# Kernel tuning notes

Measured on AMD Instinct MI355X. Metric: run time of the kernel, lower is better.

The kernel has to match this reference:

```python
import jax, jax.numpy as jnp
import numpy as np

C = 256; CM = 8; MAXI = 100; NCLS = 80
KP = (CM + 2) * CM + CM + CM * CM + CM + CM + 1  # 169 dynamic-kernel params

def _ln(x, g, b, eps=1e-5):
    m = x.mean(-1, keepdims=True)
    v = ((x - m) ** 2).mean(-1, keepdims=True)
    return g * (x - m) * jax.lax.rsqrt(v + eps) + b

def _mlp(x, hw, hb, lng, lnb, fw, fb):
    # torchvision MLP: [Linear -> LayerNorm -> SiLU] * n_hidden -> Linear
    for i in range(hw.shape[0]):
        x = jax.nn.silu(_ln(x @ hw[i] + hb[i], lng[i], lnb[i]))
    return x @ fw + fb

def _conv1x1_bn(x, w, s, b):
    # 1x1 conv (no bias) + inference-mode BatchNorm folded into per-channel affine
    y = jnp.einsum('bchw,oc->bohw', x, w)
    return y * s[None, :, None, None] + b[None, :, None, None]

def _grid(h, w):
    # normalized cell-center coordinates, (x, y) order, shape [h, w, 2]
    ys = (jnp.arange(h, dtype=jnp.float32) + 0.5) / h
    xs = (jnp.arange(w, dtype=jnp.float32) + 0.5) / w
    return jnp.stack([jnp.broadcast_to(xs[None, :], (h, w)),
                      jnp.broadcast_to(ys[:, None], (h, w))], axis=-1)

def setup_inputs() -> dict:
    key = jax.random.key(0)
    ks = iter(jax.random.split(key, 40))
    nrm = lambda shape, s=0.02: s * jax.random.normal(next(ks), shape, jnp.float32)
    B = 4
    inp = {
        'x0': jax.random.normal(next(ks), (B, 3, 512, 512), jnp.float32),
        'x1': jax.random.normal(next(ks), (B, 64, 256, 256), jnp.float32),
        'x2': jax.random.normal(next(ks), (B, 128, 128, 128), jnp.float32),
        'x3': jax.random.normal(next(ks), (B, 256, 64, 64), jnp.float32),
        'x4': jax.random.normal(next(ks), (B, 512, 32, 32), jnp.float32),
        'x5': jax.random.normal(next(ks), (B, 1024, 16, 16), jnp.float32),
        'lat3_w': nrm((C, 256)), 'lat3_s': jnp.ones((C,)), 'lat3_b': jnp.zeros((C,)),
        'lat4_w': nrm((C, 512)), 'lat4_s': jnp.ones((C,)), 'lat4_b': jnp.zeros((C,)),
        'lat5_w': nrm((C, 1024)), 'lat5_s': jnp.ones((C,)), 'lat5_b': jnp.zeros((C,)),
        'mlat_w': nrm((C, 256)), 'mlat_s': jnp.ones((C,)), 'mlat_b': jnp.zeros((C,)),
        'mhead_w': nrm((CM, C, 3, 3)), 'mhead_s': jnp.ones((CM,)), 'mhead_b': jnp.zeros((CM,)),
        'loc_hw': nrm((4, C, C)), 'loc_hb': jnp.zeros((4, C)), 'loc_lng': jnp.ones((4, C)), 'loc_lnb': jnp.zeros((4, C)),
        'loc_fw': nrm((C, 1)), 'loc_fb': -5.0 * jnp.ones((1,)),
        'cls_hw': nrm((4, C, C)), 'cls_hb': jnp.zeros((4, C)), 'cls_lng': jnp.ones((4, C)), 'cls_lnb': jnp.zeros((4, C)),
        'cls_fw': nrm((C, NCLS)), 'cls_fb': jnp.zeros((NCLS,)),
        'ker_hw': nrm((4, C, C)), 'ker_hb': jnp.zeros((4, C)), 'ker_lng': jnp.ones((4, C)), 'ker_lnb': jnp.zeros((4, C)),
        'ker_fw': nrm((C, KP)), 'ker_fb': jnp.zeros((KP,)),
    }
    return inp

def reference(x0, x1, x2, x3, x4, x5,
              lat3_w, lat3_s, lat3_b, lat4_w, lat4_s, lat4_b, lat5_w, lat5_s, lat5_b,
              mlat_w, mlat_s, mlat_b, mhead_w, mhead_s, mhead_b,
              loc_hw, loc_hb, loc_lng, loc_lnb, loc_fw, loc_fb,
              cls_hw, cls_hb, cls_lng, cls_lnb, cls_fw, cls_fb,
              ker_hw, ker_hb, ker_lng, ker_lnb, ker_fw, ker_fb):
    B, _, H, W = x0.shape
    lvls = [(x3, lat3_w, lat3_s, lat3_b), (x4, lat4_w, lat4_s, lat4_b), (x5, lat5_w, lat5_s, lat5_b)]
    feats = [_conv1x1_bn(x, w, s, b) for (x, w, s, b) in lvls]
    flat = jnp.concatenate([f.reshape(B, C, -1).transpose(0, 2, 1) for f in feats], axis=1)  # [B, L, C]
    loc_logits = _mlp(flat, loc_hw, loc_hb, loc_lng, loc_lnb, loc_fw, loc_fb)[..., 0]       # [B, L]
    top_vals, top_idx = jax.lax.top_k(loc_logits, MAXI)
    scores = jax.nn.sigmoid(top_vals)
    num_instances = (scores > 0.5).sum(axis=1)
    gfeat = jnp.take_along_axis(flat, top_idx[:, :, None], axis=1)  # [B, I, C]
    # mask branch
    mf = _conv1x1_bn(x3, mlat_w, mlat_s, mlat_b)
    mf = jax.lax.conv_general_dilated(mf, mhead_w, (1, 1), 'SAME', dimension_numbers=('NCHW', 'OIHW', 'NCHW'))
    mf = jax.nn.silu(mf * mhead_s[None, :, None, None] + mhead_b[None, :, None, None])  # [B, CM, h3, w3]
    h3, w3 = x3.shape[2], x3.shape[3]
    offs_flat = jnp.concatenate([_grid(x.shape[2], x.shape[3]).reshape(-1, 2) for x in (x3, x4, x5)], axis=0)
    offs = offs_flat[top_idx]                                # [B, I, 2]
    grid = _grid(h3, w3).transpose(2, 0, 1)                  # [2, h3, w3]
    grid = grid[None, None] - offs[:, :, :, None, None]      # [B, I, 2, h, w]
    mfi = jnp.broadcast_to(mf[:, None], (B, MAXI, CM, h3, w3))
    feats_i = jnp.concatenate([mfi, grid], axis=2)           # [B, I, CM+2, h, w]
    dyn = _mlp(gfeat, ker_hw, ker_hb, ker_lng, ker_lnb, ker_fw, ker_fb)  # [B, I, KP]
    c = CM
    o = (c + 2) * c
    w1 = dyn[..., :o].reshape(B, MAXI, c + 2, c)
    b1 = dyn[..., o:o + c].reshape(B, MAXI, c, 1, 1); o += c
    w2 = dyn[..., o:o + c * c].reshape(B, MAXI, c, c); o += c * c
    b2 = dyn[..., o:o + c].reshape(B, MAXI, c, 1, 1); o += c
    w3 = dyn[..., o:o + c].reshape(B, MAXI, c, 1); o += c
    b3 = dyn[..., o:].reshape(B, MAXI, 1, 1, 1)
    m = jax.nn.silu(jnp.einsum('bichw,bicd->bidhw', feats_i, w1) + b1)
    m = jax.nn.silu(jnp.einsum('bichw,bicd->bidhw', m, w2) + b2)
    m = jnp.einsum('bichw,bicd->bidhw', m, w3) + b3
    masks = jax.nn.sigmoid(m[:, :, 0])                       # [B, I, h3, w3]
    classes = jnp.argmax(_mlp(gfeat, cls_hw, cls_hb, cls_lng, cls_lnb, cls_fw, cls_fb), axis=-1)
    masks = jax.image.resize(masks, (B, MAXI, H, W), method='bilinear', antialias=False)
    return (num_instances, scores, classes, masks)
```

## Files before the change

kernel.cpp:

```cpp
#include <hip/hip_runtime.h>
#include <hip/hip_bf16.h>
#include <math.h>

#define DEVI __device__ __forceinline__

constexpr int LTOT  = 5376;
constexpr int NINST = 100;
constexpr int NCLS  = 80;
constexpr int KPAR  = 169;

DEVI float waveAllSum(float v) {
#pragma unroll
  for (int s = 32; s > 0; s >>= 1) v += __shfl_xor(v, s, 64);
  return v;
}
DEVI float siluf(float x) { return x / (1.0f + expf(-x)); }
DEVI float sigmf(float x) { return 1.0f / (1.0f + expf(-x)); }

__global__ __launch_bounds__(256) void wtrans(
    const float* __restrict__ w3, const float* __restrict__ w4,
    const float* __restrict__ w5, const float* __restrict__ wm,
    float* __restrict__ wt3, float* __restrict__ wt4,
    float* __restrict__ wt5, float* __restrict__ wtm)
{
  __shared__ float t[64][65];
  const int bid = blockIdx.x;
  const float* src; float* dst; int K, rel;
  if (bid < 16)       { src = w3; dst = wt3; K = 256;  rel = bid; }
  else if (bid < 48)  { src = w4; dst = wt4; K = 512;  rel = bid - 16; }
  else if (bid < 112) { src = w5; dst = wt5; K = 1024; rel = bid - 48; }
  else                { src = wm; dst = wtm; K = 256;  rel = bid - 112; }
  const int ctiles = K >> 6;
  const int ot = rel / ctiles, ct = rel % ctiles;
  const int o0 = ot * 64, c0 = ct * 64;
  const int tid = threadIdx.x;
#pragma unroll
  for (int s = 0; s < 16; ++s) {
    const int e = tid + 256*s;
    const int r = e >> 6, c = e & 63;
    t[r][c] = src[(long)(o0 + r)*K + c0 + c];
  }
  __syncthreads();
#pragma unroll
  for (int s = 0; s < 16; ++s) {
    const int e = tid + 256*s;
    const int q = e >> 6, p = e & 63;
    dst[(long)(c0 + q)*256 + o0 + p] = t[p][q];
  }
}

__global__ __launch_bounds__(256) void lateral_main(
    const float* __restrict__ x3, const float* __restrict__ x4, const float* __restrict__ x5,
    const float* __restrict__ wt3, const float* __restrict__ s3, const float* __restrict__ b3,
    const float* __restrict__ wt4, const float* __restrict__ s4, const float* __restrict__ b4,
    const float* __restrict__ wt5, const float* __restrict__ s5, const float* __restrict__ b5,
    const float* __restrict__ wtm, const float* __restrict__ sm, const float* __restrict__ bm,
    float* __restrict__ flat, float* __restrict__ mlatb)
{
  __shared__ float xs[32][36];
  __shared__ float ws[32][256];
  const int tid = threadIdx.x;
  const int rg = tid >> 6, cg = tid & 63;
  const int bid = blockIdx.x;
  const float *x, *wt, *sc, *bi;
  int K, P, b, p0, baseL = 0; bool tomlat = false;
  if (bid < 512)       { x=x3; wt=wt3; sc=s3; bi=b3; K=256;  P=4096; b=bid>>7;  p0=(bid&127)*32; }
  else if (bid < 1024) { const int rel=bid-512;  x=x3; wt=wtm; sc=sm; bi=bm; K=256;  P=4096; b=rel>>7; p0=(rel&127)*32; tomlat=true; }
  else if (bid < 1152) { const int rel=bid-1024; x=x4; wt=wt4; sc=s4; bi=b4; K=512;  P=1024; b=rel>>5; p0=(rel&31)*32; baseL=4096; }
  else                 { const int rel=bid-1152; x=x5; wt=wt5; sc=s5; bi=b5; K=1024; P=256;  b=rel>>3; p0=(rel&7)*32;  baseL=5120; }
  const float* xb = x + (long)b * K * P;
  float acc[8][4] = {};
  const int nkb = K >> 5;
  for (int kb = 0; kb < nkb; ++kb) {
    __syncthreads();
#pragma unroll
    for (int s = 0; s < 4; ++s) {
      const int e = tid + 256*s;
      const int kk = e >> 5, px = e & 31;
      xs[kk][px] = xb[(long)(kb*32 + kk)*P + p0 + px];
    }
    {
      const float4* w4p = reinterpret_cast<const float4*>(wt + (kb << 13));
#pragma unroll
      for (int q = 0; q < 8; ++q) {
        const int c = tid + (q << 8);
        *reinterpret_cast<float4*>(&ws[c >> 6][4*(c & 63)]) = w4p[c];
      }
    }
    __syncthreads();
#pragma unroll
    for (int kk = 0; kk < 32; ++kk) {
      const float4 a0 = *reinterpret_cast<const float4*>(&xs[kk][8*rg]);
      const float4 a1 = *reinterpret_cast<const float4*>(&xs[kk][8*rg+4]);
      const float ar[8] = {a0.x,a0.y,a0.z,a0.w,a1.x,a1.y,a1.z,a1.w};
      const float4 wv = *reinterpret_cast<const float4*>(&ws[kk][4*cg]);
#pragma unroll
      for (int i = 0; i < 8; ++i) {
        acc[i][0] += ar[i]*wv.x; acc[i][1] += ar[i]*wv.y;
        acc[i][2] += ar[i]*wv.z; acc[i][3] += ar[i]*wv.w;
      }
    }
  }
  const float4 sA = *reinterpret_cast<const float4*>(&sc[4*cg]);
  const float4 bA = *reinterpret_cast<const float4*>(&bi[4*cg]);
  if (!tomlat) {
#pragma unroll
    for (int i = 0; i < 8; ++i) {
      const float4 ov = { acc[i][0]*sA.x+bA.x, acc[i][1]*sA.y+bA.y,
                          acc[i][2]*sA.z+bA.z, acc[i][3]*sA.w+bA.w };
      *reinterpret_cast<float4*>(&flat[((long)b*LTOT + baseL + p0 + 8*rg + i)*256 + 4*cg]) = ov;
    }
  } else {
#pragma unroll
    for (int j = 0; j < 4; ++j) {
      const float sj = (&sA.x)[j], bj = (&bA.x)[j];
      const float4 o0 = { acc[0][j]*sj+bj, acc[1][j]*sj+bj, acc[2][j]*sj+bj, acc[3][j]*sj+bj };
      const float4 o1 = { acc[4][j]*sj+bj, acc[5][j]*sj+bj, acc[6][j]*sj+bj, acc[7][j]*sj+bj };
      float* mb = &mlatb[((long)b*256 + 4*cg + j)*4096 + p0 + 8*rg];
      *reinterpret_cast<float4*>(mb) = o0;
      *reinterpret_cast<float4*>(mb + 4) = o1;
    }
  }
}

__global__ __attribute__((amdgpu_waves_per_eu(3, 3))) __launch_bounds__(256)
void loc4(
    const float* __restrict__ in, const float* __restrict__ hw,
    const float* __restrict__ hb, const float* __restrict__ lng, const float* __restrict__ lnb,
    const float* __restrict__ fw, const float* __restrict__ fb, float* __restrict__ logits)
{
  __shared__ float xls[4][7][256];
  const int tid = threadIdx.x;
  const int rg = tid >> 6, cg = tid & 63;
  const int r0 = blockIdx.x * 28 + rg * 7;
  float* xw = &xls[rg][0][0];
#pragma unroll
  for (int i = 0; i < 7; ++i) {
    const float4 v = *reinterpret_cast<const float4*>(&in[(long)(r0 + i)*256 + 4*cg]);
    *reinterpret_cast<float4*>(&xw[i*256 + 4*cg]) = v;
  }
  const float4 fw4 = *reinterpret_cast<const float4*>(&fw[4*cg]);
  const float fbv = fb[0];

#define LOADG(W, A, g)                                                      \
  {                                                                         \
    const int kk4 = (g) << 2;                                               \
    W[0] = *reinterpret_cast<const float4*>(&w[(kk4 + 0) << 8]);            \
    W[1] = *reinterpret_cast<const float4*>(&w[(kk4 + 1) << 8]);            \
    W[2] = *reinterpret_cast<const float4*>(&w[(kk4 + 2) << 8]);            \
    W[3] = *reinterpret_cast<const float4*>(&w[(kk4 + 3) << 8]);            \
    _Pragma("unroll")                                                       \
    for (int r = 0; r < 7; ++r)                                             \
      A[r] = *reinterpret_cast<const float4*>(&xw[r*256 + kk4]);            \
  }
#define FMAG(W, A)                                                          \
  _Pragma("unroll")                                                         \
  for (int u = 0; u < 4; ++u) {                                             \
    _Pragma("unroll")                                                       \
    for (int r = 0; r < 7; ++r) {                                           \
      const float a = (&A[r].x)[u];                                         \
      acc[r][0] += a*W[u].x; acc[r][1] += a*W[u].y;                         \
      acc[r][2] += a*W[u].z; acc[r][3] += a*W[u].w;                         \
    }                                                                       \
  }

  for (int L = 0; L < 4; ++L) {
    const float* w = hw + L*65536 + 4*cg;
    float acc[7][4] = {};
    float4 wvA[4], wvB[4], avA[7], avB[7];
    LOADG(wvA, avA, 0)
    for (int g = 0; g < 64; g += 2) {
      LOADG(wvB, avB, g + 1)
      FMAG(wvA, avA)
      if (g + 2 < 64) LOADG(wvA, avA, g + 2)
      FMAG(wvB, avB)
    }
    const float4 hb4 = *reinterpret_cast<const float4*>(&hb[L*256 + 4*cg]);
    const float4 g4  = *reinterpret_cast<const float4*>(&lng[L*256 + 4*cg]);
    const float4 lb4 = *reinterpret_cast<const float4*>(&lnb[L*256 + 4*cg]);
#pragma unroll
    for (int r = 0; r < 7; ++r) {
      const float y0 = acc[r][0]+hb4.x, y1 = acc[r][1]+hb4.y;
      const float y2 = acc[r][2]+hb4.z, y3 = acc[r][3]+hb4.w;
      const float m = waveAllSum(y0+y1+y2+y3) * (1.0f/256.0f);
      const float d0=y0-m, d1=y1-m, d2=y2-m, d3=y3-m;
      const float var = waveAllSum(d0*d0+d1*d1+d2*d2+d3*d3) * (1.0f/256.0f);
      const float rs = rsqrtf(var + 1e-5f);
      const float o0 = siluf(g4.x*d0*rs + lb4.x);
      const float o1 = siluf(g4.y*d1*rs + lb4.y);
      const float o2 = siluf(g4.z*d2*rs + lb4.z);
      const float o3 = siluf(g4.w*d3*rs + lb4.w);
      if (L < 3) {
        const float4 ov = {o0, o1, o2, o3};
        *reinterpret_cast<float4*>(&xw[r*256 + 4*cg]) = ov;
      } else {
        float d = o0*fw4.x + o1*fw4.y + o2*fw4.z + o3*fw4.w;
        d = waveAllSum(d);
        if (cg == 0) logits[r0 + r] = d + fbv;
      }
    }
  }
#undef LOADG
#undef FMAG
}

__global__ __launch_bounds__(256) void topk_gather(
    const float* __restrict__ logits, const float* __restrict__ flat,
    int* __restrict__ topi, float* __restrict__ gfeat,
    float* __restrict__ dout)
{
  __shared__ float sv[LTOT];
  __shared__ float rv[4];
  __shared__ int   ri[4];
  __shared__ int   sidx[NINST];
  __shared__ int   winsh;
  const int b = blockIdx.x, tid = threadIdx.x;
  for (int l = tid; l < LTOT; l += 256) sv[l] = logits[b*LTOT + l];
  __syncthreads();
  float bvt = -INFINITY; int bit = 0x7fffffff;
  for (int l = tid; l < LTOT; l += 256) {
    const float v = sv[l];
    if (v > bvt) { bvt = v; bit = l; }
  }
  int cnt = 0;
  for (int t = 0; t < NINST; ++t) {
    float bv = bvt; int bidx = bit;
#pragma unroll
    for (int s = 32; s > 0; s >>= 1) {
      const float v2 = __shfl_xor(bv, s, 64);
      const int   i2 = __shfl_xor(bidx, s, 64);
      if (v2 > bv || (v2 == bv && i2 < bidx)) { bv = v2; bidx = i2; }
    }
    if ((tid & 63) == 0) { rv[tid >> 6] = bv; ri[tid >> 6] = bidx; }
    __syncthreads();
    if (tid == 0) {
      bv = rv[0]; bidx = ri[0];
#pragma unroll
      for (int q = 1; q < 4; ++q)
        if (rv[q] > bv || (rv[q] == bv && ri[q] < bidx)) { bv = rv[q]; bidx = ri[q]; }
      sidx[t] = bidx; topi[b*NINST + t] = bidx;
      dout[4 + b*NINST + t] = sigmf(bv);
      if (bv > 0.0f) ++cnt;
      winsh = bidx;
    }
    __syncthreads();
    const int wi = winsh;
    if (bit == wi) {
      sv[wi] = -INFINITY;
      bvt = -INFINITY; bit = 0x7fffffff;
      for (int l = tid; l < LTOT; l += 256) {
        const float v = sv[l];
        if (v > bvt) { bvt = v; bit = l; }
      }
    }
  }
  if (tid == 0) dout[b] = (float)cnt;
  __syncthreads();
  for (int t = 0; t < NINST; ++t) {
    const int ix = sidx[t];
    gfeat[((long)b*NINST + t)*256 + tid] = flat[((long)b*LTOT + ix)*256 + tid];
  }
}

__global__ __launch_bounds__(256) void clsker4(
    const float* __restrict__ gfeat, float* __restrict__ h2,
    const float* __restrict__ chw, const float* __restrict__ chb,
    const float* __restrict__ cg_, const float* __restrict__ cb_,
    const float* __restrict__ khw, const float* __restrict__ khb,
    const float* __restrict__ kg_, const float* __restrict__ kb_)
{
  __shared__ float xls[4][2][256];
  const int tid = threadIdx.x;
  const int rg = tid >> 6, cg = tid & 63;
  const bool ker = blockIdx.x >= 50;
  const int rb = (ker ? (blockIdx.x - 50) : blockIdx.x) * 8;
  const int r0 = rb + 2*rg;
  const int ob = r0 + (ker ? 400 : 0);
  const float* hw = ker ? khw : chw;
  const float* hb = ker ? khb : chb;
  const float* g_ = ker ? kg_ : cg_;
  const float* lb = ker ? kb_ : cb_;
  float* xw = &xls[rg][0][0];
#pragma unroll
  for (int i = 0; i < 2; ++i) {
    const float4 v = *reinterpret_cast<const float4*>(&gfeat[(long)(r0 + i)*256 + 4*cg]);
    *reinterpret_cast<float4*>(&xw[i*256 + 4*cg]) = v;
  }

#define LOADG2(W, A, g)                                                     \
  {                                                                         \
    const int kk4 = (g) << 2;                                               \
    W[0] = *reinterpret_cast<const float4*>(&w[(kk4 + 0) << 8]);            \
    W[1] = *reinterpret_cast<const float4*>(&w[(kk4 + 1) << 8]);            \
    W[2] = *reinterpret_cast<const float4*>(&w[(kk4 + 2) << 8]);            \
    W[3] = *reinterpret_cast<const float4*>(&w[(kk4 + 3) << 8]);            \
    A[0] = *reinterpret_cast<const float4*>(&xw[kk4]);                      \
    A[1] = *reinterpret_cast<const float4*>(&xw[256 + kk4]);                \
  }
#define FMAG2(W, A)                                                         \
  _Pragma("unroll")                                                         \
  for (int u = 0; u < 4; ++u) {                                             \
    _Pragma("unroll")                                                       \
    for (int r = 0; r < 2; ++r) {                                           \
      const float a = (&A[r].x)[u];                                         \
      acc[r][0] += a*W[u].x; acc[r][1] += a*W[u].y;                         \
      acc[r][2] += a*W[u].z; acc[r][3] += a*W[u].w;                         \
    }                                                                       \
  }

  for (int L = 0; L < 4; ++L) {
    const float* w = hw + L*65536 + 4*cg;
    float acc[2][4] = {};
    float4 wvA[4], wvB[4], avA[2], avB[2];
    LOADG2(wvA, avA, 0)
    for (int g = 0; g < 64; g += 2) {
      LOADG2(wvB, avB, g + 1)
      FMAG2(wvA, avA)
      if (g + 2 < 64) LOADG2(wvA, avA, g + 2)
      FMAG2(wvB, avB)
    }
    const float4 hb4 = *reinterpret_cast<const float4*>(&hb[L*256 + 4*cg]);
    const float4 g4  = *reinterpret_cast<const float4*>(&g_[L*256 + 4*cg]);
    const float4 lb4 = *reinterpret_cast<const float4*>(&lb[L*256 + 4*cg]);
#pragma unroll
    for (int i = 0; i < 2; ++i) {
      const float y0 = acc[i][0]+hb4.x, y1 = acc[i][1]+hb4.y;
      const float y2 = acc[i][2]+hb4.z, y3 = acc[i][3]+hb4.w;
      const float m = waveAllSum(y0+y1+y2+y3) * (1.0f/256.0f);
      const float d0=y0-m, d1=y1-m, d2=y2-m, d3=y3-m;
      const float var = waveAllSum(d0*d0+d1*d1+d2*d2+d3*d3) * (1.0f/256.0f);
      const float rs = rsqrtf(var + 1e-5f);
      const float4 ov = { siluf(g4.x*d0*rs + lb4.x), siluf(g4.y*d1*rs + lb4.y),
                          siluf(g4.z*d2*rs + lb4.z), siluf(g4.w*d3*rs + lb4.w) };
      if (L < 3) *reinterpret_cast<float4*>(&xw[i*256 + 4*cg]) = ov;
      else       *reinterpret_cast<float4*>(&h2[(long)(ob + i)*256 + 4*cg]) = ov;
    }
  }
#undef LOADG2
#undef FMAG2
}

__global__ __launch_bounds__(256) void heads(
    const float* __restrict__ h2, const float* __restrict__ cfw, const float* __restrict__ cfb,
    const float* __restrict__ kfw, const float* __restrict__ kfb,
    float* __restrict__ dout, float* __restrict__ dyn)
{
  __shared__ float xr[256];
  __shared__ float lv[NCLS];
  const int bid = blockIdx.x, tid = threadIdx.x;
  xr[tid] = h2[(long)bid*256 + tid];
  __syncthreads();
  if (bid < 400) {
    if (tid < NCLS) {
      float a0=0.f, a1=0.f, a2=0.f, a3=0.f;
      for (int k = 0; k < 256; k += 4) {
        a0 += xr[k+0]*cfw[(k+0)*NCLS + tid];
        a1 += xr[k+1]*cfw[(k+1)*NCLS + tid];
        a2 += xr[k+2]*cfw[(k+2)*NCLS + tid];
        a3 += xr[k+3]*cfw[(k+3)*NCLS + tid];
      }
      lv[tid] = (a0+a1) + (a2+a3) + cfb[tid];
    }
    __syncthreads();
    if (tid == 0) {
      float bv = lv[0]; int bi2 = 0;
      for (int o = 1; o < NCLS; ++o) if (lv[o] > bv) { bv = lv[o]; bi2 = o; }
      dout[404 + bid] = (float)bi2;
    }
  } else {
    if (tid < KPAR) {
      float a0=0.f, a1=0.f, a2=0.f, a3=0.f;
      for (int k = 0; k < 256; k += 4) {
        a0 += xr[k+0]*kfw[(k+0)*KPAR + tid];
        a1 += xr[k+1]*kfw[(k+1)*KPAR + tid];
        a2 += xr[k+2]*kfw[(k+2)*KPAR + tid];
        a3 += xr[k+3]*kfw[(k+3)*KPAR + tid];
      }
      dyn[(long)(bid-400)*KPAR + tid] = (a0+a1) + (a2+a3) + kfb[tid];
    }
  }
}

__global__ __launch_bounds__(256) void conv3(
    const float* __restrict__ mlat, const float* __restrict__ mw,
    float* __restrict__ partial)
{
  const int bid = blockIdx.x;
  const int cc = bid & 7;
  const int tile = (bid >> 3) & 15;
  const int b = bid >> 7;
  const int y0 = (tile >> 2)*16, x0 = (tile & 3)*16;
  const int tid = threadIdx.x;
  const int ly = tid >> 4, lx = tid & 15;
  __shared__ float til[2][18][19];
  __shared__ float wch[8][32][12];
  for (int e = tid; e < 2304; e += 256) {
    const int o = e / 288, rem = e % 288;
    const int c = rem / 9, qq = rem - c*9;
    wch[o][c][qq] = mw[((o*256) + cc*32 + c)*9 + qq];
  }
  int lofs[3], gofs[3], chn[3]; bool vld[3], has[3];
  float* tf = &til[0][0][0];
#pragma unroll
  for (int s = 0; s < 3; ++s) {
    const int e = tid + 256*s;
    has[s] = (e < 648);
    lofs[s] = 0; gofs[s] = 0; chn[s] = 0; vld[s] = false;
    if (has[s]) {
      const int ch = (e >= 324) ? 1 : 0;
      const int pos = e - ch*324;
      const int iy = pos / 18, ix = pos - iy*18;
      const int gy = y0 - 1 + iy, gx = x0 - 1 + ix;
      vld[s] = (gy >= 0 && gy < 64 && gx >= 0 && gx < 64);
      lofs[s] = ch*342 + iy*19 + ix;
      gofs[s] = gy*64 + gx;
      chn[s] = ch;
    }
  }
  const float* xbase = mlat + ((long)b*256 + cc*32)*4096;
  float acc[8] = {};
  for (int r = 0; r < 16; ++r) {
    __syncthreads();
#pragma unroll
    for (int s = 0; s < 3; ++s)
      if (has[s]) tf[lofs[s]] = vld[s] ? xbase[(long)(2*r + chn[s])*4096 + gofs[s]] : 0.f;
    __syncthreads();
#pragma unroll
    for (int ch = 0; ch < 2; ++ch) {
      const int c = 2*r + ch;
      float t[9];
#pragma unroll
      for (int dy = 0; dy < 3; ++dy)
#pragma unroll
        for (int dx = 0; dx < 3; ++dx) t[dy*3+dx] = til[ch][ly+dy][lx+dx];
#pragma unroll
      for (int o = 0; o < 8; ++o) {
        const float4 wa = *reinterpret_cast<const float4*>(&wch[o][c][0]);
        const float4 wb = *reinterpret_cast<const float4*>(&wch[o][c][4]);
        const float w8 = wch[o][c][8];
        acc[o] += t[0]*wa.x + t[1]*wa.y + t[2]*wa.z + t[3]*wa.w
                + t[4]*wb.x + t[5]*wb.y + t[6]*wb.z + t[7]*wb.w + t[8]*w8;
      }
    }
  }
  const long pbase = (((long)b*8 + cc)*8)*4096 + (y0+ly)*64 + (x0+lx);
#pragma unroll
  for (int o = 0; o < 8; ++o) partial[pbase + (long)o*4096] = acc[o];
}

__global__ __launch_bounds__(256) void mhead_fin(
    const float* __restrict__ partial, const float* __restrict__ s,
    const float* __restrict__ bi, float* __restrict__ mhead)
{
  const int idx = blockIdx.x*256 + threadIdx.x;
  const int p = idx & 4095;
  const int o = (idx >> 12) & 7;
  const int b = idx >> 15;
  float v = 0.f;
#pragma unroll
  for (int cc = 0; cc < 8; ++cc) v += partial[(((long)b*8 + cc)*8 + o)*4096 + p];
  v = v*s[o] + bi[o];
  mhead[idx] = siluf(v);
}

__global__ __launch_bounds__(256) void mask_fused(
    const float* __restrict__ dyn, const int* __restrict__ topi,
    const float* __restrict__ mhead, float* __restrict__ dout)
{
  __shared__ float msrc[18][64];
  __shared__ float dd[KPAR];
  __shared__ float so[2];
  const int bid = blockIdx.x;
  const int inst = bid >> 2, q = bid & 3;
  const int tid = threadIdx.x;
  if (tid < KPAR) dd[tid] = dyn[(long)inst*KPAR + tid];
  if (tid == 0) {
    const int l = topi[inst];
    float ox, oy;
    if (l < 4096)      { ox = ((l & 63) + 0.5f)*(1.f/64.f); oy = ((l >> 6) + 0.5f)*(1.f/64.f); }
    else if (l < 5120) { const int t = l - 4096; ox = ((t & 31) + 0.5f)*(1.f/32.f); oy = ((t >> 5) + 0.5f)*(1.f/32.f); }
    else               { const int t = l - 5120; ox = ((t & 15) + 0.5f)*(1.f/16.f); oy = ((t >> 4) + 0.5f)*(1.f/16.f); }
    so[0] = ox; so[1] = oy;
  }
  __syncthreads();
  const float ox = so[0], oy = so[1];
  const int b = inst / NINST;
  const float* mh = mhead + (long)b*8*4096;
  const int r0s = 16*q - 1;
  for (int e = tid; e < 1152; e += 256) {
    const int r = e >> 6, x = e & 63;
    int sy = r0s + r; sy = sy < 0 ? 0 : (sy > 63 ? 63 : sy);
    const int p = sy*64 + x;
    float f[10];
#pragma unroll
    for (int c = 0; c < 8; ++c) f[c] = mh[c*4096 + p];
    f[8] = (x + 0.5f)*(1.f/64.f) - ox;
    f[9] = (sy + 0.5f)*(1.f/64.f) - oy;
    float m1[8];
#pragma unroll
    for (int d = 0; d < 8; ++d) {
      float t = dd[80 + d];
#pragma unroll
      for (int c = 0; c < 10; ++c) t += f[c]*dd[c*8 + d];
      m1[d] = siluf(t);
    }
    float m2[8];
#pragma unroll
    for (int d = 0; d < 8; ++d) {
      float t = dd[152 + d];
#pragma unroll
      for (int c = 0; c < 8; ++c) t += m1[c]*dd[88 + c*8 + d];
      m2[d] = siluf(t);
    }
    float o = dd[168];
#pragma unroll
    for (int c = 0; c < 8; ++c) o += m2[c]*dd[160 + c];
    msrc[r][x] = sigmf(o);
  }
  __syncthreads();
  const int j4 = tid & 127;
  const int half = tid >> 7;
  const int ix0 = (j4 & 1) ? (j4 >> 1) : (j4 >> 1) - 1;
  const int xlo = ix0 < 0 ? 0 : ix0;
  const int xhi = (ix0 + 1 > 63) ? 63 : ix0 + 1;
  float fx[4];
#pragma unroll
  for (int m = 0; m < 4; ++m) {
    const int x = 4*j4 + m;
    const float tx = (x + 0.5f)*0.125f - 0.5f;
    fx[m] = tx - (float)ix0;
  }
  float* dbase = dout + 804 + ((long)inst << 18);
  for (int it = 0; it < 64; ++it) {
    const int yy = 2*it + half;
    const int y = 128*q + yy;
    const float ty = (y + 0.5f)*0.125f - 0.5f;
    const float fyf = floorf(ty);
    const int iy0 = (int)fyf;
    const float fy = ty - fyf;
    const int r0 = iy0 - r0s;
    const float L0 = msrc[r0][xlo],   R0 = msrc[r0][xhi];
    const float L1 = msrc[r0+1][xlo], R1 = msrc[r0+1][xhi];
    const float L = L0 + (L1 - L0)*fy;
    const float R = R0 + (R1 - R0)*fy;
    const float4 ovv = { L + (R - L)*fx[0], L + (R - L)*fx[1],
                         L + (R - L)*fx[2], L + (R - L)*fx[3] };
    *reinterpret_cast<float4*>(&dbase[((long)y << 9) + (j4 << 2)]) = ovv;
  }
}

extern "C" void kernel_launch(void* const* d_in, const int* in_sizes, int n_in,
                              void* d_out, int out_size, void* d_ws, size_t ws_size,
                              hipStream_t stream)
{
  (void)in_sizes; (void)n_in; (void)out_size; (void)ws_size;
  const float* x3      = (const float*)d_in[3];
  const float* x4      = (const float*)d_in[4];
  const float* x5      = (const float*)d_in[5];
  const float* lat3_w  = (const float*)d_in[6];
  const float* lat3_s  = (const float*)d_in[7];
  const float* lat3_b  = (const float*)d_in[8];
  const float* lat4_w  = (const float*)d_in[9];
  const float* lat4_s  = (const float*)d_in[10];
  const float* lat4_b  = (const float*)d_in[11];
  const float* lat5_w  = (const float*)d_in[12];
  const float* lat5_s  = (const float*)d_in[13];
  const float* lat5_b  = (const float*)d_in[14];
  const float* mlat_w  = (const float*)d_in[15];
  const float* mlat_s  = (const float*)d_in[16];
  const float* mlat_b  = (const float*)d_in[17];
  const float* mhead_w = (const float*)d_in[18];
  const float* mhead_s = (const float*)d_in[19];
  const float* mhead_b = (const float*)d_in[20];
  const float* loc_hw  = (const float*)d_in[21];
  const float* loc_hb  = (const float*)d_in[22];
  const float* loc_lng = (const float*)d_in[23];
  const float* loc_lnb = (const float*)d_in[24];
  const float* loc_fw  = (const float*)d_in[25];
  const float* loc_fb  = (const float*)d_in[26];
  const float* cls_hw  = (const float*)d_in[27];
  const float* cls_hb  = (const float*)d_in[28];
  const float* cls_lng = (const float*)d_in[29];
  const float* cls_lnb = (const float*)d_in[30];
  const float* cls_fw  = (const float*)d_in[31];
  const float* cls_fb  = (const float*)d_in[32];
  const float* ker_hw  = (const float*)d_in[33];
  const float* ker_hb  = (const float*)d_in[34];
  const float* ker_lng = (const float*)d_in[35];
  const float* ker_lnb = (const float*)d_in[36];
  const float* ker_fw  = (const float*)d_in[37];
  const float* ker_fb  = (const float*)d_in[38];

  float* ws      = (float*)d_ws;
  float* flat    = ws;
  float* mlatb   = ws + 5505024;
  float* partial = ws + 9699328;
  float* mheadb  = ws + 10747904;
  float* h2      = ws + 10878976;
  float* logits  = ws + 11083776;
  int*   topi    = (int*)(ws + 11105280);
  float* gfeat   = ws + 11105680;
  float* dynb    = ws + 11208080;
  float* wt3     = ws + 11275680;
  float* wt4     = ws + 11341216;
  float* wt5     = ws + 11472288;
  float* wtm     = ws + 11734432;
  float* dout    = (float*)d_out;

  wtrans<<<128, 256, 0, stream>>>(lat3_w, lat4_w, lat5_w, mlat_w, wt3, wt4, wt5, wtm);
  lateral_main<<<1184, 256, 0, stream>>>(x3, x4, x5,
      wt3, lat3_s, lat3_b, wt4, lat4_s, lat4_b, wt5, lat5_s, lat5_b,
      wtm, mlat_s, mlat_b, flat, mlatb);
  conv3<<<512, 256, 0, stream>>>(mlatb, mhead_w, partial);
  mhead_fin<<<512, 256, 0, stream>>>(partial, mhead_s, mhead_b, mheadb);
  loc4<<<768, 256, 0, stream>>>(flat, loc_hw, loc_hb, loc_lng, loc_lnb,
                                loc_fw, loc_fb, logits);
  topk_gather<<<4, 256, 0, stream>>>(logits, flat, topi, gfeat, dout);
  clsker4<<<100, 256, 0, stream>>>(gfeat, h2,
      cls_hw, cls_hb, cls_lng, cls_lnb, ker_hw, ker_hb, ker_lng, ker_lnb);
  heads<<<800, 256, 0, stream>>>(h2, cls_fw, cls_fb, ker_fw, ker_fb, dout, dynb);
  mask_fused<<<1600, 256, 0, stream>>>(dynb, topi, mheadb, dout);
}
```

Before: 793.0 us.

## Fold mask lateral 1x1 conv+BN into 3x3 mask head weights

Precomputes combined weights by composing the mask lateral 1x1 conv and its BN affine into the 3x3 mask-head conv, so conv3 reads x3 directly. This removes the 512 lateral_main blocks that produced the mlat buffer, along with its write and read traffic. The folded BN bias is added in mhead_fin as a border-aware sum of per-tap biases, which keeps zero-padding semantics exact. It adds a small weight-prep step and a slight change in floating-point rounding order.

```diff
diff --git a/kernel.cpp b/kernel.cpp
--- a/kernel.cpp
+++ b/kernel.cpp
@@ -17,23 +17,37 @@
 DEVI float siluf(float x) { return x / (1.0f + expf(-x)); }
 DEVI float sigmf(float x) { return 1.0f / (1.0f + expf(-x)); }
 
-__global__ __launch_bounds__(256) void wtrans(
+__global__ __launch_bounds__(256) void wprep(
     const float* __restrict__ w3, const float* __restrict__ w4,
-    const float* __restrict__ w5, const float* __restrict__ wm,
-    float* __restrict__ wt3, float* __restrict__ wt4,
-    float* __restrict__ wt5, float* __restrict__ wtm)
+    const float* __restrict__ w5,
+    const float* __restrict__ mlat_w, const float* __restrict__ mlat_s,
+    const float* __restrict__ mlat_b, const float* __restrict__ mhead_w,
+    float* __restrict__ wt3, float* __restrict__ wt4, float* __restrict__ wt5,
+    float* __restrict__ wc, float* __restrict__ Bt)
 {
   __shared__ float t[64][65];
   const int bid = blockIdx.x;
+  const int tid = threadIdx.x;
+  if (bid >= 112) {
+    const int rel = bid - 112;
+    const int o = rel / 9, q = rel % 9;
+    float acc = 0.f, bacc = 0.f;
+    for (int c = 0; c < 256; ++c) {
+      const float mh = mhead_w[((o << 8) + c)*9 + q];
+      acc  += mh * mlat_s[c] * mlat_w[(c << 8) + tid];
+      bacc += mh * mlat_b[c];
+    }
+    wc[((o << 8) + tid)*9 + q] = acc;
+    if (tid == 0) Bt[rel] = bacc;
+    return;
+  }
   const float* src; float* dst; int K, rel;
   if (bid < 16)       { src = w3; dst = wt3; K = 256;  rel = bid; }
   else if (bid < 48)  { src = w4; dst = wt4; K = 512;  rel = bid - 16; }
-  else if (bid < 112) { src = w5; dst = wt5; K = 1024; rel = bid - 48; }
-  else                { src = wm; dst = wtm; K = 256;  rel = bid - 112; }
+  else                { src = w5; dst = wt5; K = 1024; rel = bid - 48; }
   const int ctiles = K >> 6;
   const int ot = rel / ctiles, ct = rel % ctiles;
   const int o0 = ot * 64, c0 = ct * 64;
-  const int tid = threadIdx.x;
 #pragma unroll
   for (int s = 0; s < 16; ++s) {
     const int e = tid + 256*s;
@@ -54,8 +68,7 @@
     const float* __restrict__ wt3, const float* __restrict__ s3, const float* __restrict__ b3,
     const float* __restrict__ wt4, const float* __restrict__ s4, const float* __restrict__ b4,
     const float* __restrict__ wt5, const float* __restrict__ s5, const float* __restrict__ b5,
-    const float* __restrict__ wtm, const float* __restrict__ sm, const float* __restrict__ bm,
-    float* __restrict__ flat, float* __restrict__ mlatb)
+    float* __restrict__ flat)
 {
   __shared__ float xs[32][36];
   __shared__ float ws[32][256];
@@ -63,11 +76,10 @@
   const int rg = tid >> 6, cg = tid & 63;
   const int bid = blockIdx.x;
   const float *x, *wt, *sc, *bi;
-  int K, P, b, p0, baseL = 0; bool tomlat = false;
-  if (bid < 512)       { x=x3; wt=wt3; sc=s3; bi=b3; K=256;  P=4096; b=bid>>7;  p0=(bid&127)*32; }
-  else if (bid < 1024) { const int rel=bid-512;  x=x3; wt=wtm; sc=sm; bi=bm; K=256;  P=4096; b=rel>>7; p0=(rel&127)*32; tomlat=true; }
-  else if (bid < 1152) { const int rel=bid-1024; x=x4; wt=wt4; sc=s4; bi=b4; K=512;  P=1024; b=rel>>5; p0=(rel&31)*32; baseL=4096; }
-  else                 { const int rel=bid-1152; x=x5; wt=wt5; sc=s5; bi=b5; K=1024; P=256;  b=rel>>3; p0=(rel&7)*32;  baseL=5120; }
+  int K, P, b, p0, baseL = 0;
+  if (bid < 512)      { x=x3; wt=wt3; sc=s3; bi=b3; K=256;  P=4096; b=bid>>7;  p0=(bid&127)*32; }
+  else if (bid < 640) { const int rel=bid-512; x=x4; wt=wt4; sc=s4; bi=b4; K=512;  P=1024; b=rel>>5; p0=(rel&31)*32; baseL=4096; }
+  else                { const int rel=bid-640; x=x5; wt=wt5; sc=s5; bi=b5; K=1024; P=256;  b=rel>>3; p0=(rel&7)*32;  baseL=5120; }
   const float* xb = x + (long)b * K * P;
   float acc[8][4] = {};
   const int nkb = K >> 5;
@@ -103,23 +115,11 @@
   }
   const float4 sA = *reinterpret_cast<const float4*>(&sc[4*cg]);
   const float4 bA = *reinterpret_cast<const float4*>(&bi[4*cg]);
-  if (!tomlat) {
-#pragma unroll
-    for (int i = 0; i < 8; ++i) {
-      const float4 ov = { acc[i][0]*sA.x+bA.x, acc[i][1]*sA.y+bA.y,
-                          acc[i][2]*sA.z+bA.z, acc[i][3]*sA.w+bA.w };
-      *reinterpret_cast<float4*>(&flat[((long)b*LTOT + baseL + p0 + 8*rg + i)*256 + 4*cg]) = ov;
-    }
-  } else {
-#pragma unroll
-    for (int j = 0; j < 4; ++j) {
-      const float sj = (&sA.x)[j], bj = (&bA.x)[j];
-      const float4 o0 = { acc[0][j]*sj+bj, acc[1][j]*sj+bj, acc[2][j]*sj+bj, acc[3][j]*sj+bj };
-      const float4 o1 = { acc[4][j]*sj+bj, acc[5][j]*sj+bj, acc[6][j]*sj+bj, acc[7][j]*sj+bj };
-      float* mb = &mlatb[((long)b*256 + 4*cg + j)*4096 + p0 + 8*rg];
-      *reinterpret_cast<float4*>(mb) = o0;
-      *reinterpret_cast<float4*>(mb + 4) = o1;
-    }
+#pragma unroll
+  for (int i = 0; i < 8; ++i) {
+    const float4 ov = { acc[i][0]*sA.x+bA.x, acc[i][1]*sA.y+bA.y,
+                        acc[i][2]*sA.z+bA.z, acc[i][3]*sA.w+bA.w };
+    *reinterpret_cast<float4*>(&flat[((long)b*LTOT + baseL + p0 + 8*rg + i)*256 + 4*cg]) = ov;
   }
 }
 
@@ -382,7 +382,7 @@
 }
 
 __global__ __launch_bounds__(256) void conv3(
-    const float* __restrict__ mlat, const float* __restrict__ mw,
+    const float* __restrict__ x3, const float* __restrict__ wc,
     float* __restrict__ partial)
 {
   const int bid = blockIdx.x;
@@ -397,7 +397,7 @@
   for (int e = tid; e < 2304; e += 256) {
     const int o = e / 288, rem = e % 288;
     const int c = rem / 9, qq = rem - c*9;
-    wch[o][c][qq] = mw[((o*256) + cc*32 + c)*9 + qq];
+    wch[o][c][qq] = wc[((o*256) + cc*32 + c)*9 + qq];
   }
   int lofs[3], gofs[3], chn[3]; bool vld[3], has[3];
   float* tf = &til[0][0][0];
@@ -417,7 +417,7 @@
       chn[s] = ch;
     }
   }
-  const float* xbase = mlat + ((long)b*256 + cc*32)*4096;
+  const float* xbase = x3 + ((long)b*256 + cc*32)*4096;
   float acc[8] = {};
   for (int r = 0; r < 16; ++r) {
     __syncthreads();
@@ -449,16 +449,23 @@
 }
 
 __global__ __launch_bounds__(256) void mhead_fin(
-    const float* __restrict__ partial, const float* __restrict__ s,
-    const float* __restrict__ bi, float* __restrict__ mhead)
+    const float* __restrict__ partial, const float* __restrict__ Bt,
+    const float* __restrict__ s, const float* __restrict__ bi,
+    float* __restrict__ mhead)
 {
   const int idx = blockIdx.x*256 + threadIdx.x;
   const int p = idx & 4095;
   const int o = (idx >> 12) & 7;
   const int b = idx >> 15;
+  const int y = p >> 6, x = p & 63;
   float v = 0.f;
 #pragma unroll
   for (int cc = 0; cc < 8; ++cc) v += partial[(((long)b*8 + cc)*8 + o)*4096 + p];
+#pragma unroll
+  for (int q = 0; q < 9; ++q) {
+    const int sy = y + q/3 - 1, sx = x + q%3 - 1;
+    if (sy >= 0 && sy < 64 && sx >= 0 && sx < 64) v += Bt[o*9 + q];
+  }
   v = v*s[o] + bi[o];
   mhead[idx] = siluf(v);
 }
@@ -593,26 +600,26 @@
 
   float* ws      = (float*)d_ws;
   float* flat    = ws;
-  float* mlatb   = ws + 5505024;
-  float* partial = ws + 9699328;
-  float* mheadb  = ws + 10747904;
-  float* h2      = ws + 10878976;
-  float* logits  = ws + 11083776;
-  int*   topi    = (int*)(ws + 11105280);
-  float* gfeat   = ws + 11105680;
-  float* dynb    = ws + 11208080;
-  float* wt3     = ws + 11275680;
-  float* wt4     = ws + 11341216;
-  float* wt5     = ws + 11472288;
-  float* wtm     = ws + 11734432;
+  float* wc      = ws + 5505024;
+  float* Bt      = ws + 5523456;
+  float* partial = ws + 5523528;
+  float* mheadb  = ws + 6572104;
+  float* h2      = ws + 6703176;
+  float* logits  = ws + 6907976;
+  int*   topi    = (int*)(ws + 6929480);
+  float* gfeat   = ws + 6929880;
+  float* dynb    = ws + 7032280;
+  float* wt3     = ws + 7099880;
+  float* wt4     = ws + 7165416;
+  float* wt5     = ws + 7296488;
   float* dout    = (float*)d_out;
 
-  wtrans<<<128, 256, 0, stream>>>(lat3_w, lat4_w, lat5_w, mlat_w, wt3, wt4, wt5, wtm);
-  lateral_main<<<1184, 256, 0, stream>>>(x3, x4, x5,
-      wt3, lat3_s, lat3_b, wt4, lat4_s, lat4_b, wt5, lat5_s, lat5_b,
-      wtm, mlat_s, mlat_b, flat, mlatb);
-  conv3<<<512, 256, 0, stream>>>(mlatb, mhead_w, partial);
-  mhead_fin<<<512, 256, 0, stream>>>(partial, mhead_s, mhead_b, mheadb);
+  wprep<<<184, 256, 0, stream>>>(lat3_w, lat4_w, lat5_w,
+      mlat_w, mlat_s, mlat_b, mhead_w, wt3, wt4, wt5, wc, Bt);
+  lateral_main<<<672, 256, 0, stream>>>(x3, x4, x5,
+      wt3, lat3_s, lat3_b, wt4, lat4_s, lat4_b, wt5, lat5_s, lat5_b, flat);
+  conv3<<<512, 256, 0, stream>>>(x3, wc, partial);
+  mhead_fin<<<512, 256, 0, stream>>>(partial, Bt, mhead_s, mhead_b, mheadb);
   loc4<<<768, 256, 0, stream>>>(flat, loc_hw, loc_hb, loc_lng, loc_lnb,
                                 loc_fw, loc_fb, logits);
   topk_gather<<<4, 256, 0, stream>>>(logits, flat, topi, gfeat, dout);
```

Measured after the change: 799.4 us. No clear change (+0.8%).
